# Kernel tuning notes

Measured on AMD Instinct MI355X. Metric: run time of the kernel, lower is better.

Reference implementation:

```python
import jax, jax.numpy as jnp
import numpy as np
from jax import lax

RADIUS = (3, 3, 3)  # box-filter kernel size per spatial axis (named 'radius' in source)
EPS = 1e-6


def box_sum_3d(x, ksizes=RADIUS):
    # Separable box-filter local SUM, equivalent to conv3d with an all-ones
    # (1,1,3,3,3) kernel and padding='same'.
    for ax_idx, k in enumerate(ksizes):
        kshape = [1, 1, 1, 1, 1]
        kshape[2 + ax_idx] = k
        kern = jnp.ones(kshape, dtype=x.dtype)
        x = lax.conv_general_dilated(
            x, kern, window_strides=(1, 1, 1), padding='SAME',
            dimension_numbers=('NCDHW', 'OIDHW', 'NCDHW'))
    return x


def image_gradient_3d(image):
    # torch.gradient: central differences interior, one-sided at boundaries.
    gz, gy, gx = jnp.gradient(image, axis=(2, 3, 4))
    return jnp.concatenate([gz, gy, gx], axis=1)  # [B,3,D,H,W]


def setup_inputs() -> dict:
    key = jax.random.key(0)
    k1, k2, k3, k4 = jax.random.split(key, 4)
    shape = (1, 1, 256, 256, 256)
    moving_image = jax.random.normal(k1, shape, dtype=jnp.float32)
    fixed_image = jax.random.normal(k2, shape, dtype=jnp.float32)
    moving_mask = jax.random.bernoulli(k3, 0.5, shape)
    fixed_mask = jax.random.bernoulli(k4, 0.5, shape)
    return {"moving_image": moving_image, "fixed_image": fixed_image,
            "moving_mask": moving_mask, "fixed_mask": fixed_mask}


def reference(moving_image, fixed_image, moving_mask, fixed_mask):
    npix = float(np.prod(RADIUS))  # 27

    sum_m = box_sum_3d(moving_image)
    sum_f = box_sum_3d(fixed_image)
    sum_mm = box_sum_3d(moving_image * moving_image)
    sum_ff = box_sum_3d(fixed_image * fixed_image)
    sum_mf = box_sum_3d(moving_image * fixed_image)

    moving_mean = sum_m / npix
    fixed_mean = sum_f / npix

    var_m = sum_mm - 2 * moving_mean * sum_m + npix * moving_mean * moving_mean
    var_f = sum_ff - 2 * fixed_mean * sum_f + npix * fixed_mean * fixed_mean
    var_mf = var_m * var_f
    cross = sum_mf - fixed_mean * sum_m - moving_mean * sum_f + npix * moving_mean * fixed_mean

    # dual-force total gradient: masked moving grad + masked fixed grad, halved
    grad_moving = image_gradient_3d(moving_image) * moving_mask.astype(moving_image.dtype)
    grad_fixed = image_gradient_3d(fixed_image) * fixed_mask.astype(fixed_image.dtype)
    total_grad = (grad_moving + grad_fixed) * 0.5  # [B,3,D,H,W]

    moving_mean_centered = moving_image - moving_mean
    fixed_mean_centered = fixed_image - fixed_mean
    factor = (2.0 * cross / (var_mf + EPS)
              * (moving_mean_centered - cross / (var_f * fixed_mean_centered + EPS)))

    # (cross_correlation / metric are only printed in the original, not returned)
    return -1.0 * factor * total_grad
```

## Files before the change

### kernel.cpp

```cpp
#include <hip/hip_runtime.h>


constexpr int DIM    = 256;
constexpr int PLANE  = DIM * DIM;
constexpr int NVOX   = DIM * DIM * DIM;
constexpr int TILE_X = 62;
constexpr int TILE_Y = 8;
constexpr int CHUNK_Z = 32;
constexpr float EPSF = 1e-6f;

__global__ __launch_bounds__(512) void ncc_forces(
    const float* __restrict__ M, const float* __restrict__ F,
    const int* __restrict__ maskM, const int* __restrict__ maskF,
    float* __restrict__ out)
{
    const int tx = threadIdx.x;
    const int ty = threadIdx.y;
    const int x  = blockIdx.x * TILE_X - 1 + tx;
    const int y  = blockIdx.y * TILE_Y + ty;
    const int z0 = blockIdx.z * CHUNK_Z;

    const bool xok      = (unsigned)x < (unsigned)DIM;
    const bool do_store = (tx >= 1) && (tx <= TILE_X) && (x < DIM);
    const int laneL = (tx == 0)  ? 0  : tx - 1;
    const int laneR = (tx == 63) ? 63 : tx + 1;
    const bool yUok = (y - 1) >= 0;
    const bool yDok = (y + 1) < DIM;

    float Pm0=0.f,Pf0=0.f,Pmm0=0.f,Pff0=0.f,Pmf0=0.f;
    float Pm1=0.f,Pf1=0.f,Pmm1=0.f,Pff1=0.f,Pmf1=0.f;
    float mcA=0.f, mcB=0.f, fcA=0.f, fcB=0.f;
    float gxm_p=0.f, gym_p=0.f, gxf_p=0.f, gyf_p=0.f;

    for (int s = 0; s <= CHUNK_Z + 1; ++s) {
        const int  zl  = z0 - 1 + s;
        const bool zok = (unsigned)zl < (unsigned)DIM;

        float mU=0.f, mC=0.f, mD=0.f, fU=0.f, fC=0.f, fD=0.f;
        if (zok && xok) {
            const int rowC = zl * PLANE + y * DIM + x;
            mC = M[rowC]; fC = F[rowC];
            if (yUok) { mU = M[rowC - DIM]; fU = F[rowC - DIM]; }
            if (yDok) { mD = M[rowC + DIM]; fD = F[rowC + DIM]; }
        }

        const float mUL=__shfl(mU,laneL), mUR=__shfl(mU,laneR);
        const float mCL=__shfl(mC,laneL), mCR=__shfl(mC,laneR);
        const float mDL=__shfl(mD,laneL), mDR=__shfl(mD,laneR);
        const float fUL=__shfl(fU,laneL), fUR=__shfl(fU,laneR);
        const float fCL=__shfl(fC,laneL), fCR=__shfl(fC,laneR);
        const float fDL=__shfl(fD,laneL), fDR=__shfl(fD,laneR);

        const float Pm2  = (mUL+mU+mUR)+(mCL+mC+mCR)+(mDL+mD+mDR);
        const float Pf2  = (fUL+fU+fUR)+(fCL+fC+fCR)+(fDL+fD+fDR);
        const float Pmm2 = (mUL*mUL+mU*mU+mUR*mUR)+(mCL*mCL+mC*mC+mCR*mCR)+(mDL*mDL+mD*mD+mDR*mDR);
        const float Pff2 = (fUL*fUL+fU*fU+fUR*fUR)+(fCL*fCL+fC*fC+fCR*fCR)+(fDL*fDL+fD*fD+fDR*fDR);
        const float Pmf2 = (mUL*fUL+mU*fU+mUR*fUR)+(mCL*fCL+mC*fC+mCR*fCR)+(mDL*fDL+mD*fD+mDR*fDR);

        const float gxm = (x==0) ? (mCR-mC) : (x==DIM-1) ? (mC-mCL) : 0.5f*(mCR-mCL);
        const float gxf = (x==0) ? (fCR-fC) : (x==DIM-1) ? (fC-fCL) : 0.5f*(fCR-fCL);
        const float gym = (y==0) ? (mD-mC) : (y==DIM-1) ? (mC-mU) : 0.5f*(mD-mU);
        const float gyf = (y==0) ? (fD-fC) : (y==DIM-1) ? (fC-fU) : 0.5f*(fD-fU);

        if (s >= 2 && do_store) {
            const int zo = zl - 1;

            const float sum_m  = Pm0  + Pm1  + Pm2;
            const float sum_f  = Pf0  + Pf1  + Pf2;
            const float sum_mm = Pmm0 + Pmm1 + Pmm2;
            const float sum_ff = Pff0 + Pff1 + Pff2;
            const float sum_mf = Pmf0 + Pmf1 + Pmf2;

            const float moving_mean = sum_m / 27.0f;
            const float fixed_mean  = sum_f / 27.0f;
            const float var_m = sum_mm - 2.0f*moving_mean*sum_m + 27.0f*moving_mean*moving_mean;
            const float var_f = sum_ff - 2.0f*fixed_mean*sum_f  + 27.0f*fixed_mean*fixed_mean;
            const float var_mf = var_m * var_f;
            const float cross = sum_mf - fixed_mean*sum_m - moving_mean*sum_f
                                + 27.0f*moving_mean*fixed_mean;
            const float mmc = mcB - moving_mean;
            const float fmc = fcB - fixed_mean;
            const float factor = 2.0f * cross / (var_mf + EPSF)
                                 * (mmc - cross / (var_f * fmc + EPSF));

            const float gzm = (zo==0) ? (mC - mcB) : (zo==DIM-1) ? (mcB - mcA) : 0.5f*(mC - mcA);
            const float gzf = (zo==0) ? (fC - fcB) : (zo==DIM-1) ? (fcB - fcA) : 0.5f*(fC - fcA);

            const int idx = zo * PLANE + y * DIM + x;
            const float wm = maskM[idx] ? 1.0f : 0.0f;
            const float wf = maskF[idx] ? 1.0f : 0.0f;

            const float tgz = 0.5f*(gzm  *wm + gzf  *wf);
            const float tgy = 0.5f*(gym_p*wm + gyf_p*wf);
            const float tgx = 0.5f*(gxm_p*wm + gxf_p*wf);

            out[idx]          = -factor * tgz;
            out[NVOX + idx]   = -factor * tgy;
            out[2*NVOX + idx] = -factor * tgx;
        }

        Pm0=Pm1;  Pf0=Pf1;  Pmm0=Pmm1; Pff0=Pff1; Pmf0=Pmf1;
        Pm1=Pm2;  Pf1=Pf2;  Pmm1=Pmm2; Pff1=Pff2; Pmf1=Pmf2;
        mcA=mcB;  mcB=mC;   fcA=fcB;   fcB=fC;
        gxm_p=gxm; gym_p=gym; gxf_p=gxf; gyf_p=gyf;
    }
}

extern "C" void kernel_launch(void* const* d_in, const int* in_sizes, int n_in,
                              void* d_out, int out_size, void* d_ws, size_t ws_size,
                              hipStream_t stream) {
    const float* M  = (const float*)d_in[0];
    const float* F  = (const float*)d_in[1];
    const int* mm   = (const int*)d_in[2];
    const int* fm   = (const int*)d_in[3];
    float* out      = (float*)d_out;

    dim3 block(64, TILE_Y, 1);
    dim3 grid((DIM + TILE_X - 1) / TILE_X,
              DIM / TILE_Y,
              DIM / CHUNK_Z);
    hipLaunchKernelGGL(ncc_forces, grid, block, 0, stream, M, F, mm, fm, out);
}
```

Baseline: 465.3 us.

## Vectorize to float4 per lane covering full rows, with nontemporal stores

Each 64-lane wavefront now covers a full 256-wide row, with every lane handling four consecutive voxels through float4 loads. This removes the overlapping x-halo tiles and their redundant loads, and the x-direction box sum and gradient need only two shuffles per quantity. Outputs go out as nontemporal vector stores, masks are read as int4, the z loop is fully unrolled with ring-buffer slots, and block and chunk sizes change. The cost is higher register pressure from the float4 ring buffers, which may reduce occupancy.

```diff
diff --git a/kernel.cpp b/kernel.cpp
--- a/kernel.cpp
+++ b/kernel.cpp
@@ -1,108 +1,165 @@
 #include <hip/hip_runtime.h>
 
 
-constexpr int DIM    = 256;
-constexpr int PLANE  = DIM * DIM;
-constexpr int NVOX   = DIM * DIM * DIM;
-constexpr int TILE_X = 62;
-constexpr int TILE_Y = 8;
-constexpr int CHUNK_Z = 32;
-constexpr float EPSF = 1e-6f;
+constexpr int DIM     = 256;
+constexpr int PLANE   = DIM * DIM;
+constexpr int NVOX    = DIM * DIM * DIM;
+constexpr int CHUNK_Z = 16;
+constexpr int BY      = 4;
+constexpr float EPSF  = 1e-6f;
 
-__global__ __launch_bounds__(512) void ncc_forces(
+typedef float nvec4 __attribute__((ext_vector_type(4)));
+
+__device__ __forceinline__ float shlz(float v) {
+    float r = __shfl_up(v, 1);
+    return (threadIdx.x == 0) ? 0.f : r;
+}
+__device__ __forceinline__ float shrz(float v) {
+    float r = __shfl_down(v, 1);
+    return (threadIdx.x == 63) ? 0.f : r;
+}
+__device__ __forceinline__ float4 add3(const float4& a, const float4& b, const float4& c) {
+    return make_float4(a.x+b.x+c.x, a.y+b.y+c.y, a.z+b.z+c.z, a.w+b.w+c.w);
+}
+__device__ __forceinline__ float4 prod3(const float4& a, const float4& b,
+                                        const float4& c, const float4& d,
+                                        const float4& e, const float4& f) {
+    return make_float4(a.x*b.x + c.x*d.x + e.x*f.x,
+                       a.y*b.y + c.y*d.y + e.y*f.y,
+                       a.z*b.z + c.z*d.z + e.z*f.z,
+                       a.w*b.w + c.w*d.w + e.w*f.w);
+}
+__device__ __forceinline__ float4 sub4(const float4& a, const float4& b) {
+    return make_float4(a.x-b.x, a.y-b.y, a.z-b.z, a.w-b.w);
+}
+__device__ __forceinline__ float4 scl4(const float4& a, float s) {
+    return make_float4(a.x*s, a.y*s, a.z*s, a.w*s);
+}
+__device__ __forceinline__ float4 xsum3(const float4& c) {
+    float l = shlz(c.w), r = shrz(c.x);
+    return make_float4(l + c.x + c.y, c.x + c.y + c.z, c.y + c.z + c.w, c.z + c.w + r);
+}
+__device__ __forceinline__ void ntstore4(float* p, const float4& v) {
+    nvec4 t; t.x = v.x; t.y = v.y; t.z = v.z; t.w = v.w;
+    __builtin_nontemporal_store(t, (nvec4*)p);
+}
+
+__device__ __forceinline__ void pw1(
+    float sum_m, float sum_f, float sum_mm, float sum_ff, float sum_mf,
+    float mA, float mB, float mN,
+    float fA, float fB, float fN,
+    int zflag,
+    float gx_m, float gy_m, float gx_f, float gy_f,
+    int km, int kf,
+    float& o0, float& o1, float& o2)
+{
+    float mmean = sum_m / 27.0f;
+    float fmean = sum_f / 27.0f;
+    float var_m = sum_mm - 2.f*mmean*sum_m + 27.f*mmean*mmean;
+    float var_f = sum_ff - 2.f*fmean*sum_f + 27.f*fmean*fmean;
+    float cross = sum_mf - fmean*sum_m - mmean*sum_f + 27.f*mmean*fmean;
+    float mmc = mB - mmean, fmc = fB - fmean;
+    float factor = 2.f * cross / (var_m*var_f + EPSF)
+                   * (mmc - cross / (var_f*fmc + EPSF));
+    float gzm = (zflag < 0) ? (mN - mB) : ((zflag > 0) ? (mB - mA) : 0.5f*(mN - mA));
+    float gzf = (zflag < 0) ? (fN - fB) : ((zflag > 0) ? (fB - fA) : 0.5f*(fN - fA));
+    float wm = km ? 1.f : 0.f, wf = kf ? 1.f : 0.f;
+    float nf = -0.5f * factor;
+    o0 = nf * (gzm*wm + gzf*wf);
+    o1 = nf * (gy_m*wm + gy_f*wf);
+    o2 = nf * (gx_m*wm + gx_f*wf);
+}
+
+__global__ __launch_bounds__(64 * BY) void ncc_forces(
     const float* __restrict__ M, const float* __restrict__ F,
     const int* __restrict__ maskM, const int* __restrict__ maskF,
     float* __restrict__ out)
 {
-    const int tx = threadIdx.x;
-    const int ty = threadIdx.y;
-    const int x  = blockIdx.x * TILE_X - 1 + tx;
-    const int y  = blockIdx.y * TILE_Y + ty;
+    const int y  = blockIdx.y * BY + threadIdx.y;
     const int z0 = blockIdx.z * CHUNK_Z;
+    const int xb = threadIdx.x * 4;
+    const bool yUok = (y > 0), yDok = (y < DIM - 1);
 
-    const bool xok      = (unsigned)x < (unsigned)DIM;
-    const bool do_store = (tx >= 1) && (tx <= TILE_X) && (x < DIM);
-    const int laneL = (tx == 0)  ? 0  : tx - 1;
-    const int laneR = (tx == 63) ? 63 : tx + 1;
-    const bool yUok = (y - 1) >= 0;
-    const bool yDok = (y + 1) < DIM;
+    float4 Pm[3], Pf[3], Pmm[3], Pff[3], Pmf[3];
+    float4 mc[3], fc[3];
+    float4 gxm_p, gym_p, gxf_p, gyf_p;
 
-    float Pm0=0.f,Pf0=0.f,Pmm0=0.f,Pff0=0.f,Pmf0=0.f;
-    float Pm1=0.f,Pf1=0.f,Pmm1=0.f,Pff1=0.f,Pmf1=0.f;
-    float mcA=0.f, mcB=0.f, fcA=0.f, fcB=0.f;
-    float gxm_p=0.f, gym_p=0.f, gxf_p=0.f, gyf_p=0.f;
+    auto ingest = [&](int slot, int zl, float4& gxm, float4& gym, float4& gxf, float4& gyf) {
+        const float4 z4 = make_float4(0.f, 0.f, 0.f, 0.f);
+        float4 mU = z4, mC = z4, mD = z4, fU = z4, fC = z4, fD = z4;
+        if ((unsigned)zl < (unsigned)DIM) {
+            const float* pm = M + (size_t)zl * PLANE + (size_t)y * DIM + xb;
+            const float* pf = F + (size_t)zl * PLANE + (size_t)y * DIM + xb;
+            mC = *(const float4*)pm;  fC = *(const float4*)pf;
+            if (yUok) { mU = *(const float4*)(pm - DIM); fU = *(const float4*)(pf - DIM); }
+            if (yDok) { mD = *(const float4*)(pm + DIM); fD = *(const float4*)(pf + DIM); }
+        }
+        float4 Cm  = add3(mU, mC, mD);
+        float4 Cf  = add3(fU, fC, fD);
+        float4 Cmm = prod3(mU, mU, mC, mC, mD, mD);
+        float4 Cff = prod3(fU, fU, fC, fC, fD, fD);
+        float4 Cmf = prod3(mU, fU, mC, fC, mD, fD);
+        Pm[slot]  = xsum3(Cm);
+        Pf[slot]  = xsum3(Cf);
+        Pmm[slot] = xsum3(Cmm);
+        Pff[slot] = xsum3(Cff);
+        Pmf[slot] = xsum3(Cmf);
+        mc[slot] = mC; fc[slot] = fC;
+        float mL = shlz(mC.w), mR = shrz(mC.x);
+        float fL = shlz(fC.w), fR = shrz(fC.x);
+        gxm = make_float4((threadIdx.x == 0)  ? (mC.y - mC.x) : 0.5f*(mC.y - mL),
+                          0.5f*(mC.z - mC.x),
+                          0.5f*(mC.w - mC.y),
+                          (threadIdx.x == 63) ? (mC.w - mC.z) : 0.5f*(mR - mC.z));
+        gxf = make_float4((threadIdx.x == 0)  ? (fC.y - fC.x) : 0.5f*(fC.y - fL),
+                          0.5f*(fC.z - fC.x),
+                          0.5f*(fC.w - fC.y),
+                          (threadIdx.x == 63) ? (fC.w - fC.z) : 0.5f*(fR - fC.z));
+        gym = (y == 0) ? sub4(mD, mC) : (y == DIM-1) ? sub4(mC, mU) : scl4(sub4(mD, mU), 0.5f);
+        gyf = (y == 0) ? sub4(fD, fC) : (y == DIM-1) ? sub4(fC, fU) : scl4(sub4(fD, fU), 0.5f);
+    };
 
-    for (int s = 0; s <= CHUNK_Z + 1; ++s) {
-        const int  zl  = z0 - 1 + s;
-        const bool zok = (unsigned)zl < (unsigned)DIM;
+    { float4 d0, d1, d2, d3; ingest(0, z0 - 1, d0, d1, d2, d3); }
+    ingest(1, z0, gxm_p, gym_p, gxf_p, gyf_p);
 
-        float mU=0.f, mC=0.f, mD=0.f, fU=0.f, fC=0.f, fD=0.f;
-        if (zok && xok) {
-            const int rowC = zl * PLANE + y * DIM + x;
-            mC = M[rowC]; fC = F[rowC];
-            if (yUok) { mU = M[rowC - DIM]; fU = F[rowC - DIM]; }
-            if (yDok) { mD = M[rowC + DIM]; fD = F[rowC + DIM]; }
-        }
+    #pragma unroll
+    for (int s = 2; s < CHUNK_Z + 2; ++s) {
+        const int i2 = s % 3, i1 = (s + 2) % 3, i0 = (s + 1) % 3;
+        float4 gxm, gym, gxf, gyf;
+        ingest(i2, z0 - 1 + s, gxm, gym, gxf, gyf);
 
-        const float mUL=__shfl(mU,laneL), mUR=__shfl(mU,laneR);
-        const float mCL=__shfl(mC,laneL), mCR=__shfl(mC,laneR);
-        const float mDL=__shfl(mD,laneL), mDR=__shfl(mD,laneR);
-        const float fUL=__shfl(fU,laneL), fUR=__shfl(fU,laneR);
-        const float fCL=__shfl(fC,laneL), fCR=__shfl(fC,laneR);
-        const float fDL=__shfl(fD,laneL), fDR=__shfl(fD,laneR);
+        const int zo = z0 + s - 2;
+        const int zflag = (zo == 0) ? -1 : ((zo == DIM - 1) ? 1 : 0);
+        const size_t idx = (size_t)zo * PLANE + (size_t)y * DIM + xb;
 
-        const float Pm2  = (mUL+mU+mUR)+(mCL+mC+mCR)+(mDL+mD+mDR);
-        const float Pf2  = (fUL+fU+fUR)+(fCL+fC+fCR)+(fDL+fD+fDR);
-        const float Pmm2 = (mUL*mUL+mU*mU+mUR*mUR)+(mCL*mCL+mC*mC+mCR*mCR)+(mDL*mDL+mD*mD+mDR*mDR);
-        const float Pff2 = (fUL*fUL+fU*fU+fUR*fUR)+(fCL*fCL+fC*fC+fCR*fCR)+(fDL*fDL+fD*fD+fDR*fDR);
-        const float Pmf2 = (mUL*fUL+mU*fU+mUR*fUR)+(mCL*fCL+mC*fC+mCR*fCR)+(mDL*fDL+mD*fD+mDR*fDR);
+        int4 km = *(const int4*)(maskM + idx);
+        int4 kf = *(const int4*)(maskF + idx);
 
-        const float gxm = (x==0) ? (mCR-mC) : (x==DIM-1) ? (mC-mCL) : 0.5f*(mCR-mCL);
-        const float gxf = (x==0) ? (fCR-fC) : (x==DIM-1) ? (fC-fCL) : 0.5f*(fCR-fCL);
-        const float gym = (y==0) ? (mD-mC) : (y==DIM-1) ? (mC-mU) : 0.5f*(mD-mU);
-        const float gyf = (y==0) ? (fD-fC) : (y==DIM-1) ? (fC-fU) : 0.5f*(fD-fU);
+        float4 sm  = add3(Pm[i0],  Pm[i1],  Pm[i2]);
+        float4 sf  = add3(Pf[i0],  Pf[i1],  Pf[i2]);
+        float4 smm = add3(Pmm[i0], Pmm[i1], Pmm[i2]);
+        float4 sff = add3(Pff[i0], Pff[i1], Pff[i2]);
+        float4 smf = add3(Pmf[i0], Pmf[i1], Pmf[i2]);
 
-        if (s >= 2 && do_store) {
-            const int zo = zl - 1;
+        float4 o0, o1, o2;
+        pw1(sm.x, sf.x, smm.x, sff.x, smf.x, mc[i0].x, mc[i1].x, mc[i2].x,
+            fc[i0].x, fc[i1].x, fc[i2].x, zflag, gxm_p.x, gym_p.x, gxf_p.x, gyf_p.x,
+            km.x, kf.x, o0.x, o1.x, o2.x);
+        pw1(sm.y, sf.y, smm.y, sff.y, smf.y, mc[i0].y, mc[i1].y, mc[i2].y,
+            fc[i0].y, fc[i1].y, fc[i2].y, zflag, gxm_p.y, gym_p.y, gxf_p.y, gyf_p.y,
+            km.y, kf.y, o0.y, o1.y, o2.y);
+        pw1(sm.z, sf.z, smm.z, sff.z, smf.z, mc[i0].z, mc[i1].z, mc[i2].z,
+            fc[i0].z, fc[i1].z, fc[i2].z, zflag, gxm_p.z, gym_p.z, gxf_p.z, gyf_p.z,
+            km.z, kf.z, o0.z, o1.z, o2.z);
+        pw1(sm.w, sf.w, smm.w, sff.w, smf.w, mc[i0].w, mc[i1].w, mc[i2].w,
+            fc[i0].w, fc[i1].w, fc[i2].w, zflag, gxm_p.w, gym_p.w, gxf_p.w, gyf_p.w,
+            km.w, kf.w, o0.w, o1.w, o2.w);
 
-            const float sum_m  = Pm0  + Pm1  + Pm2;
-            const float sum_f  = Pf0  + Pf1  + Pf2;
-            const float sum_mm = Pmm0 + Pmm1 + Pmm2;
-            const float sum_ff = Pff0 + Pff1 + Pff2;
-            const float sum_mf = Pmf0 + Pmf1 + Pmf2;
+        ntstore4(out + idx,            o0);
+        ntstore4(out + NVOX + idx,     o1);
+        ntstore4(out + 2 * NVOX + idx, o2);
 
-            const float moving_mean = sum_m / 27.0f;
-            const float fixed_mean  = sum_f / 27.0f;
-            const float var_m = sum_mm - 2.0f*moving_mean*sum_m + 27.0f*moving_mean*moving_mean;
-            const float var_f = sum_ff - 2.0f*fixed_mean*sum_f  + 27.0f*fixed_mean*fixed_mean;
-            const float var_mf = var_m * var_f;
-            const float cross = sum_mf - fixed_mean*sum_m - moving_mean*sum_f
-                                + 27.0f*moving_mean*fixed_mean;
-            const float mmc = mcB - moving_mean;
-            const float fmc = fcB - fixed_mean;
-            const float factor = 2.0f * cross / (var_mf + EPSF)
-                                 * (mmc - cross / (var_f * fmc + EPSF));
-
-            const float gzm = (zo==0) ? (mC - mcB) : (zo==DIM-1) ? (mcB - mcA) : 0.5f*(mC - mcA);
-            const float gzf = (zo==0) ? (fC - fcB) : (zo==DIM-1) ? (fcB - fcA) : 0.5f*(fC - fcA);
-
-            const int idx = zo * PLANE + y * DIM + x;
-            const float wm = maskM[idx] ? 1.0f : 0.0f;
-            const float wf = maskF[idx] ? 1.0f : 0.0f;
-
-            const float tgz = 0.5f*(gzm  *wm + gzf  *wf);
-            const float tgy = 0.5f*(gym_p*wm + gyf_p*wf);
-            const float tgx = 0.5f*(gxm_p*wm + gxf_p*wf);
-
-            out[idx]          = -factor * tgz;
-            out[NVOX + idx]   = -factor * tgy;
-            out[2*NVOX + idx] = -factor * tgx;
-        }
-
-        Pm0=Pm1;  Pf0=Pf1;  Pmm0=Pmm1; Pff0=Pff1; Pmf0=Pmf1;
-        Pm1=Pm2;  Pf1=Pf2;  Pmm1=Pmm2; Pff1=Pff2; Pmf1=Pmf2;
-        mcA=mcB;  mcB=mC;   fcA=fcB;   fcB=fC;
-        gxm_p=gxm; gym_p=gym; gxf_p=gxf; gyf_p=gyf;
+        gxm_p = gxm; gym_p = gym; gxf_p = gxf; gyf_p = gyf;
     }
 }
 
@@ -115,9 +172,7 @@
     const int* fm   = (const int*)d_in[3];
     float* out      = (float*)d_out;
 
-    dim3 block(64, TILE_Y, 1);
-    dim3 grid((DIM + TILE_X - 1) / TILE_X,
-              DIM / TILE_Y,
-              DIM / CHUNK_Z);
+    dim3 block(64, BY, 1);
+    dim3 grid(1, DIM / BY, DIM / CHUNK_Z);
     hipLaunchKernelGGL(ncc_forces, grid, block, 0, stream, M, F, mm, fm, out);
 }
```

After: 404.3 us. 13.1% less time.
